# Performance work log

Hardware: AMD Instinct MI355X
Metric: run time of the kernel (lower is better)

## Reference

```python
import jax, jax.numpy as jnp
import numpy as np
from jax import lax

FPLANE = 64
T = 8          # num_segments
HEADS = 4
EPS = 1e-5


def _conv2d(x, w, b):
    # x: [N,C,H,W], w: [O,I,kh,kw]
    y = lax.conv_general_dilated(x, w, (1, 1), 'SAME',
                                 dimension_numbers=('NCHW', 'OIHW', 'NCHW'))
    return y + b[None, :, None, None]


def _conv3d_grouped(x, w, b, groups):
    # x: [N,C,D,H,W], w: [O, C//groups, kd,kh,kw]
    y = lax.conv_general_dilated(x, w, (1, 1, 1), 'SAME',
                                 dimension_numbers=('NCDHW', 'OIDHW', 'NCDHW'),
                                 feature_group_count=groups)
    return y + b[None, :, None, None, None]


def setup_inputs() -> dict:
    key = jax.random.key(0)
    ks = jax.random.split(key, 5)
    N, C, H, W = T * 16, FPLANE, 56, 56
    x = jax.random.normal(ks[0], (N, C, H, W), dtype=jnp.float32)
    attn_w = jax.random.normal(ks[1], (HEADS, C, 3, 3), dtype=jnp.float32) * 0.05
    attn_b = jax.random.normal(ks[2], (HEADS,), dtype=jnp.float32) * 0.05
    bn_gamma = jnp.ones((C,), dtype=jnp.float32)
    bn_beta = jnp.zeros((C,), dtype=jnp.float32)
    conv3d_w = jax.random.normal(ks[3], (2, C // 2, 3, 3, 3), dtype=jnp.float32) * 0.05
    conv3d_b = jax.random.normal(ks[4], (2,), dtype=jnp.float32) * 0.05
    return {'x': x, 'attn_w': attn_w, 'attn_b': attn_b,
            'bn_gamma': bn_gamma, 'bn_beta': bn_beta,
            'conv3d_w': conv3d_w, 'conv3d_b': conv3d_b}


def reference(x, attn_w, attn_b, bn_gamma, bn_beta, conv3d_w, conv3d_b):
    N, C, H, W = x.shape
    B = N // T
    half = C // 2
    quarter = C // 4

    # spatial attention: conv2d -> ReLU -> Sigmoid, per-head gating
    attn = jax.nn.sigmoid(jax.nn.relu(_conv2d(x, attn_w, attn_b)))  # [N,HEADS,H,W]
    xh = x.reshape(N, HEADS, C // HEADS, H, W) * attn[:, :, None]
    x2 = xh.reshape(N, C, H, W)

    # [B*T,C,H,W] -> [B,C,T,H,W]
    x5 = x2.reshape(B, T, C, H, W).transpose(0, 2, 1, 3, 4)

    # BatchNorm3d (training-mode batch statistics) + ReLU
    mean = jnp.mean(x5, axis=(0, 2, 3, 4), keepdims=True)
    var = jnp.var(x5, axis=(0, 2, 3, 4), keepdims=True)
    x_bn = (x5 - mean) * lax.rsqrt(var + EPS)
    x_bn = x_bn * bn_gamma[None, :, None, None, None] + bn_beta[None, :, None, None, None]
    x_bn_relu = jax.nn.relu(x_bn)

    # grouped conv3d gate (2 groups, 1 output channel each), tanh
    gate = jnp.tanh(_conv3d_grouped(x_bn_relu, conv3d_w, conv3d_b, groups=2))  # [B,2,T,H,W]
    g1 = gate[:, 0:1]
    g2 = gate[:, 1:2]

    x_g1 = x5[:, :half]
    x_g2 = x5[:, half:]
    y1 = g1 * x_g1
    y2 = g2 * x_g2
    r1 = x_g1 - y1
    r2 = x_g2 - y2

    pad_t = ((0, 0), (0, 0), (0, 1), (0, 0), (0, 0))
    pad_b = ((0, 0), (0, 0), (1, 0), (0, 0), (0, 0))
    y1 = jnp.pad(y1[:, :, 1:], pad_t) + r1   # left shift in time, zero pad
    y2 = jnp.pad(y2[:, :, :-1], pad_b) + r2  # right shift in time, zero pad

    # interleave sub-halves: view [B,2,C/4,T,H,W] -> permute -> [B,C/2,T,H,W]
    def interleave(y):
        return (y.reshape(B, 2, quarter, T, H, W)
                 .transpose(0, 2, 1, 3, 4, 5)
                 .reshape(B, half, T, H, W))

    y = jnp.concatenate([interleave(y1), interleave(y2)], axis=1)  # [B,C,T,H,W]
    return y.transpose(0, 2, 1, 3, 4).reshape(N, C, H, W)
```

## Files before the change

kernel.cpp:

```cpp
#include <hip/hip_runtime.h>
#include <hip/hip_bf16.h>

#define HW 3136
#define CTOT 64
#define NTOT 128
#define BB 16
#define TTT 8

static __device__ __forceinline__ float bf2f(unsigned short u) {
    union { unsigned int ui; float f; } v;
    v.ui = ((unsigned int)u) << 16;
    return v.f;
}
static __device__ __forceinline__ unsigned short f2bf(float f) {
    union { float f; unsigned int u; } v;
    v.f = f;
    unsigned int u = v.u;
    unsigned int r = (u + 0x7fffu + ((u >> 16) & 1u)) >> 16;
    return (unsigned short)r;
}

__global__ __launch_bounds__(128) void k_attn(const float* __restrict__ x,
                                              const float* __restrict__ aw,
                                              const float* __restrict__ ab,
                                              float* __restrict__ attn,
                                              unsigned short* __restrict__ x2,
                                              float* __restrict__ stats) {
    const int tile = blockIdx.x % 49;
    const int n = blockIdx.x / 49;
    const int chunk = threadIdx.x >> 4;
    const int qi = threadIdx.x & 15;
    const int quad = tile * 16 + qi;
    const int q = quad % 14;
    const int h = quad / 14;
    const int w0 = q * 4;

    __shared__ float wl[2304];
    __shared__ float l[8][16][17];
    __shared__ float4 abuf[4][16];

    const float* xn = x + (size_t)n * CTOT * HW;
    const int c0 = chunk * 8;

    auto loadrows = [&](int c, float r[3][6]) {
#pragma unroll
        for (int dh = 0; dh < 3; ++dh) {
            const int hh = h + dh - 1;
            const bool v = (hh >= 0) && (hh < 56);
            const float* row = xn + c * HW + (v ? hh : h) * 56 + w0;
            const float m = v ? 1.f : 0.f;
            const float4 mid = *(const float4*)row;
            const float e0 = row[(q > 0) ? -1 : 0] * ((q > 0) ? m : 0.f);
            const float e5 = row[(q < 13) ? 4 : 3] * ((q < 13) ? m : 0.f);
            r[dh][0] = e0;
            r[dh][1] = mid.x * m; r[dh][2] = mid.y * m;
            r[dh][3] = mid.z * m; r[dh][4] = mid.w * m;
            r[dh][5] = e5;
        }
    };

    float bufA[3][6], bufB[3][6];
    loadrows(c0, bufA);

#pragma unroll
    for (int i = 0; i < 18; ++i) {
        const int idx = threadIdx.x + i * 128;
        const int hd = idx & 3;
        const int kw = (idx >> 2) % 3;
        const int dh = (idx / 12) % 3;
        const int c = idx / 36;
        wl[idx] = aw[hd * 576 + c * 9 + dh * 3 + kw];
    }
    __syncthreads();

    float acc[4][4];
#pragma unroll
    for (int hd = 0; hd < 4; ++hd)
#pragma unroll
        for (int j = 0; j < 4; ++j) acc[hd][j] = 0.f;

    float midst[8][4];

#pragma unroll
    for (int i = 0; i < 8; ++i) {
        float (*cur)[6] = (i & 1) ? bufB : bufA;
        float (*nxt)[6] = (i & 1) ? bufA : bufB;
        if (i < 7) loadrows(c0 + i + 1, nxt);

        midst[i][0] = cur[1][1]; midst[i][1] = cur[1][2];
        midst[i][2] = cur[1][3]; midst[i][3] = cur[1][4];

        const int c = c0 + i;
#pragma unroll
        for (int dh = 0; dh < 3; ++dh) {
            const float* wb = &wl[c * 36 + dh * 12];
            const float4 wk0 = *(const float4*)(wb);
            const float4 wk1 = *(const float4*)(wb + 4);
            const float4 wk2 = *(const float4*)(wb + 8);
#pragma unroll
            for (int j = 0; j < 4; ++j) {
                const float a0 = cur[dh][j], a1 = cur[dh][j + 1], a2 = cur[dh][j + 2];
                acc[0][j] = fmaf(a0, wk0.x, fmaf(a1, wk1.x, fmaf(a2, wk2.x, acc[0][j])));
                acc[1][j] = fmaf(a0, wk0.y, fmaf(a1, wk1.y, fmaf(a2, wk2.y, acc[1][j])));
                acc[2][j] = fmaf(a0, wk0.z, fmaf(a1, wk1.z, fmaf(a2, wk2.z, acc[2][j])));
                acc[3][j] = fmaf(a0, wk0.w, fmaf(a1, wk1.w, fmaf(a2, wk2.w, acc[3][j])));
            }
        }
    }

    float* mine = &l[chunk][qi][0];
#pragma unroll
    for (int hd = 0; hd < 4; ++hd)
#pragma unroll
        for (int j = 0; j < 4; ++j) mine[hd * 4 + j] = acc[hd][j];
    __syncthreads();

    if (threadIdx.x < 64) {
        const int hd = threadIdx.x >> 4;
        const int rq = threadIdx.x & 15;
        float s0 = ab[hd], s1 = s0, s2 = s0, s3 = s0;
#pragma unroll
        for (int cch = 0; cch < 8; ++cch) {
            const float* p = &l[cch][rq][hd * 4];
            s0 += p[0]; s1 += p[1]; s2 += p[2]; s3 += p[3];
        }
        float4 o;
        o.x = s0 > 0.f ? 1.f / (1.f + __expf(-s0)) : 0.5f;
        o.y = s1 > 0.f ? 1.f / (1.f + __expf(-s1)) : 0.5f;
        o.z = s2 > 0.f ? 1.f / (1.f + __expf(-s2)) : 0.5f;
        o.w = s3 > 0.f ? 1.f / (1.f + __expf(-s3)) : 0.5f;
        *(float4*)(attn + (size_t)(n * 4 + hd) * HW + (tile * 16 + rq) * 4) = o;
        abuf[hd][rq] = o;
    }
    __syncthreads();

    const int head = chunk >> 1;
    const float4 a4 = abuf[head][qi];
    float s[8], sq[8];
#pragma unroll
    for (int i = 0; i < 8; ++i) {
        const float v0 = midst[i][0] * a4.x;
        const float v1 = midst[i][1] * a4.y;
        const float v2 = midst[i][2] * a4.z;
        const float v3 = midst[i][3] * a4.w;
        ushort4 o;
        o.x = f2bf(v0); o.y = f2bf(v1); o.z = f2bf(v2); o.w = f2bf(v3);
        *(ushort4*)(x2 + (size_t)(n * 64 + c0 + i) * HW + quad * 4) = o;
        s[i] = v0 + v1 + v2 + v3;
        sq[i] = v0 * v0 + v1 * v1 + v2 * v2 + v3 * v3;
    }
#pragma unroll
    for (int i = 0; i < 8; ++i) { mine[i] = s[i]; mine[8 + i] = sq[i]; }
    __syncthreads();
    {
        const int ch2 = threadIdx.x >> 4;
        const int k = threadIdx.x & 15;
        float t = 0.f;
#pragma unroll
        for (int qq = 0; qq < 16; ++qq) t += l[ch2][qq][k];
        const int cc = ch2 * 8 + (k & 7);
        const int rep = blockIdx.x & 15;
        atomicAdd(&stats[rep * 128 + (k >> 3) * 64 + cc], t);
    }
}

__global__ void k_finalize(const float* __restrict__ stats,
                           const float* __restrict__ gamma,
                           const float* __restrict__ beta,
                           float* __restrict__ ss) {
    const int c = threadIdx.x;
    float S = 0.f, Q = 0.f;
#pragma unroll
    for (int r = 0; r < 16; ++r) {
        S += stats[r * 128 + c];
        Q += stats[r * 128 + 64 + c];
    }
    const float cnt = 401408.0f;
    const float mean = S / cnt;
    const float var = Q / cnt - mean * mean;
    const float scale = gamma[c] * rsqrtf(var + 1e-5f);
    ss[c] = scale;
    ss[64 + c] = beta[c] - mean * scale;
}

__global__ __launch_bounds__(128) void k_conv3d(const unsigned short* __restrict__ x2,
                                                const float* __restrict__ ss,
                                                const float* __restrict__ w3,
                                                const float* __restrict__ b3,
                                                float* __restrict__ gate) {
    const int tile = blockIdx.x % 49;
    const int oc = (blockIdx.x / 49) & 1;
    const int b = blockIdx.x / 98;
    const int chunk = threadIdx.x >> 4;
    const int qi = threadIdx.x & 15;
    const int quad = tile * 16 + qi;
    const int q = quad % 14;
    const int h = quad / 14;
    const int w0 = q * 4;

    float acc[8][4];
#pragma unroll
    for (int t = 0; t < 8; ++t)
#pragma unroll
        for (int j = 0; j < 4; ++j) acc[t][j] = 0.f;

    const int ic0 = chunk * 4;
    for (int ic = ic0; ic < ic0 + 4; ++ic) {
        const int c = oc * 32 + ic;
        const float sc = ss[c], sh = ss[64 + c];
        const unsigned short* cbase = x2 + (size_t)(b * 8 * 64 + c) * HW;
        const float* wic = w3 + c * 27;
#pragma unroll
        for (int tt = 0; tt < 8; ++tt) {
            const unsigned short* plane = cbase + (size_t)tt * (64 * HW);
            float f[3][6];
#pragma unroll
            for (int dh = 0; dh < 3; ++dh) {
                const int hh = h + dh - 1;
                const bool vld = (hh >= 0) && (hh < 56);
                const unsigned short* row = plane + (vld ? hh : h) * 56 + w0;
                const float m = vld ? 1.f : 0.f;
                const float mL = (q > 0) ? m : 0.f;
                const float mR = (q < 13) ? m : 0.f;
                const ushort4 mid = *(const ushort4*)row;
                const unsigned short e0 = row[(q > 0) ? -1 : 0];
                const unsigned short e5 = row[(q < 13) ? 4 : 3];
                f[dh][0] = fmaxf(fmaf(bf2f(e0),    sc, sh), 0.f) * mL;
                f[dh][1] = fmaxf(fmaf(bf2f(mid.x), sc, sh), 0.f) * m;
                f[dh][2] = fmaxf(fmaf(bf2f(mid.y), sc, sh), 0.f) * m;
                f[dh][3] = fmaxf(fmaf(bf2f(mid.z), sc, sh), 0.f) * m;
                f[dh][4] = fmaxf(fmaf(bf2f(mid.w), sc, sh), 0.f) * m;
                f[dh][5] = fmaxf(fmaf(bf2f(e5),    sc, sh), 0.f) * mR;
            }
#pragma unroll
            for (int dh = 0; dh < 3; ++dh) {
#pragma unroll
                for (int dt = 0; dt < 3; ++dt) {
                    const int t = tt + 1 - dt;
                    if (t < 0 || t > 7) continue;
                    const float* wp = wic + dt * 9 + dh * 3;
                    const float wa = wp[0], wb = wp[1], wc = wp[2];
                    acc[t][0] = fmaf(f[dh][0], wa, fmaf(f[dh][1], wb, fmaf(f[dh][2], wc, acc[t][0])));
                    acc[t][1] = fmaf(f[dh][1], wa, fmaf(f[dh][2], wb, fmaf(f[dh][3], wc, acc[t][1])));
                    acc[t][2] = fmaf(f[dh][2], wa, fmaf(f[dh][3], wb, fmaf(f[dh][4], wc, acc[t][2])));
                    acc[t][3] = fmaf(f[dh][3], wa, fmaf(f[dh][4], wb, fmaf(f[dh][5], wc, acc[t][3])));
                }
            }
        }
    }

    __shared__ float4 l4[8 * 16 * 9];
    float4* mine = &l4[(chunk * 16 + qi) * 9];
#pragma unroll
    for (int t = 0; t < 8; ++t) {
        float4 v;
        v.x = acc[t][0]; v.y = acc[t][1]; v.z = acc[t][2]; v.w = acc[t][3];
        mine[t] = v;
    }
    __syncthreads();

    const int rt = threadIdx.x >> 4;
    const int rq = threadIdx.x & 15;
    float4 s = l4[(0 * 16 + rq) * 9 + rt];
#pragma unroll
    for (int c = 1; c < 8; ++c) {
        const float4 v = l4[(c * 16 + rq) * 9 + rt];
        s.x += v.x; s.y += v.y; s.z += v.z; s.w += v.w;
    }
    const float bb = b3[oc];
    float4 o;
    o.x = tanhf(s.x + bb);
    o.y = tanhf(s.y + bb);
    o.z = tanhf(s.z + bb);
    o.w = tanhf(s.w + bb);
    const int outquad = tile * 16 + rq;
    *(float4*)(gate + (size_t)((b * 2 + oc) * 8 + rt) * HW + outquad * 4) = o;
}

__global__ __launch_bounds__(448) void k_final(const float* __restrict__ x,
                                               const float* __restrict__ attn,
                                               const float* __restrict__ gate,
                                               float* __restrict__ out) {
    const int hg = blockIdx.x & 1;
    const int h = (blockIdx.x >> 1) % 56;
    const int b = blockIdx.x / 112;
    const int q = threadIdx.x % 14;
    const int col = threadIdx.x / 14;
    const int co = hg * 32 + col;
    const int sp = h * 56 + q * 4;

    int cs;
    if (co < 32) {
        cs = ((co & 1) << 4) | (co >> 1);
    } else {
        const int cc = co - 32;
        cs = 32 + (((cc & 1) << 4) | (cc >> 1));
    }
    const int grp = hg;
    const int head = cs >> 4;

    float4 x2v[8], g[8];
#pragma unroll
    for (int t = 0; t < 8; ++t) {
        const int n = b * 8 + t;
        const float4 xv = *(const float4*)(x + (size_t)(n * 64 + cs) * HW + sp);
        const float4 av = *(const float4*)(attn + (size_t)(n * 4 + head) * HW + sp);
        const float4 gv = *(const float4*)(gate + (size_t)((b * 2 + grp) * 8 + t) * HW + sp);
        x2v[t].x = xv.x * av.x;
        x2v[t].y = xv.y * av.y;
        x2v[t].z = xv.z * av.z;
        x2v[t].w = xv.w * av.w;
        g[t] = gv;
    }
#pragma unroll
    for (int t = 0; t < 8; ++t) {
        float4 o;
        o.x = x2v[t].x * (1.f - g[t].x);
        o.y = x2v[t].y * (1.f - g[t].y);
        o.z = x2v[t].z * (1.f - g[t].z);
        o.w = x2v[t].w * (1.f - g[t].w);
        if (grp == 0) {
            if (t < 7) {
                o.x += x2v[t + 1].x * g[t + 1].x;
                o.y += x2v[t + 1].y * g[t + 1].y;
                o.z += x2v[t + 1].z * g[t + 1].z;
                o.w += x2v[t + 1].w * g[t + 1].w;
            }
        } else {
            if (t > 0) {
                o.x += x2v[t - 1].x * g[t - 1].x;
                o.y += x2v[t - 1].y * g[t - 1].y;
                o.z += x2v[t - 1].z * g[t - 1].z;
                o.w += x2v[t - 1].w * g[t - 1].w;
            }
        }
        *(float4*)(out + (size_t)((b * 8 + t) * 64 + co) * HW + sp) = o;
    }
}

extern "C" void kernel_launch(void* const* d_in, const int* in_sizes, int n_in,
                              void* d_out, int out_size, void* d_ws, size_t ws_size,
                              hipStream_t stream) {
    const float* x = (const float*)d_in[0];
    const float* aw = (const float*)d_in[1];
    const float* ab = (const float*)d_in[2];
    const float* gamma = (const float*)d_in[3];
    const float* beta = (const float*)d_in[4];
    const float* w3 = (const float*)d_in[5];
    const float* b3 = (const float*)d_in[6];
    float* out = (float*)d_out;

    char* ws = (char*)d_ws;
    unsigned short* x2 = (unsigned short*)ws;
    float* attn = (float*)(ws + 51380224);
    float* gate = (float*)(ws + 57802752);
    float* stats = (float*)(ws + 57802752);
    float* ss = (float*)(ws + 61014528);

    hipMemsetAsync(stats, 0, 8192, stream);
    k_attn<<<6272, 128, 0, stream>>>(x, aw, ab, attn, x2, stats);
    k_finalize<<<1, 64, 0, stream>>>(stats, gamma, beta, ss);
    k_conv3d<<<1568, 128, 0, stream>>>(x2, ss, w3, b3, gate);
    k_final<<<1792, 448, 0, stream>>>(x, attn, gate, out);
}
```

Baseline: 391.8 us.

## Fold BN finalize into attn kernel, pre-apply BN+ReLU pass, LDS weights in conv3d

The BN statistics finalize moves into the tail of the attention kernel using a last-block atomic counter, which removes one kernel launch. A new elementwise kernel applies BN scale/shift and ReLU to the bf16 x2 buffer in place, so conv3d reads values that are already normalized. Conv3d then caches its weights in LDS and skips out-of-range rows instead of masking them. The cost is an extra full read and write pass over x2 (about 51 MB) plus a second bf16 rounding of the normalized values, which may not pay back the per-element ALU saved in conv3d.

```diff
diff --git a/kernel.cpp b/kernel.cpp
--- a/kernel.cpp
+++ b/kernel.cpp
@@ -23,9 +23,13 @@
 __global__ __launch_bounds__(128) void k_attn(const float* __restrict__ x,
                                               const float* __restrict__ aw,
                                               const float* __restrict__ ab,
+                                              const float* __restrict__ gamma,
+                                              const float* __restrict__ beta,
                                               float* __restrict__ attn,
                                               unsigned short* __restrict__ x2,
-                                              float* __restrict__ stats) {
+                                              float* __restrict__ stats,
+                                              unsigned int* __restrict__ counter,
+                                              float* __restrict__ ss) {
     const int tile = blockIdx.x % 49;
     const int n = blockIdx.x / 49;
     const int chunk = threadIdx.x >> 4;
@@ -162,29 +166,49 @@
         const int rep = blockIdx.x & 15;
         atomicAdd(&stats[rep * 128 + (k >> 3) * 64 + cc], t);
     }
-}
-
-__global__ void k_finalize(const float* __restrict__ stats,
-                           const float* __restrict__ gamma,
-                           const float* __restrict__ beta,
-                           float* __restrict__ ss) {
-    const int c = threadIdx.x;
-    float S = 0.f, Q = 0.f;
-#pragma unroll
-    for (int r = 0; r < 16; ++r) {
-        S += stats[r * 128 + c];
-        Q += stats[r * 128 + 64 + c];
-    }
-    const float cnt = 401408.0f;
-    const float mean = S / cnt;
-    const float var = Q / cnt - mean * mean;
-    const float scale = gamma[c] * rsqrtf(var + 1e-5f);
-    ss[c] = scale;
-    ss[64 + c] = beta[c] - mean * scale;
+
+    __syncthreads();
+    __shared__ unsigned int winflag;
+    if (threadIdx.x == 0) {
+        __threadfence();
+        winflag = (atomicAdd(counter, 1u) == gridDim.x - 1) ? 1u : 0u;
+    }
+    __syncthreads();
+    if (winflag && threadIdx.x < 64) {
+        const int c = threadIdx.x;
+        float S = 0.f, Q = 0.f;
+#pragma unroll
+        for (int r = 0; r < 16; ++r) {
+            S += atomicAdd(&stats[r * 128 + c], 0.f);
+            Q += atomicAdd(&stats[r * 128 + 64 + c], 0.f);
+        }
+        const float cnt = 401408.0f;
+        const float mean = S / cnt;
+        const float var = Q / cnt - mean * mean;
+        const float scale = gamma[c] * rsqrtf(var + 1e-5f);
+        ss[c] = scale;
+        ss[64 + c] = beta[c] - mean * scale;
+    }
+}
+
+__global__ __launch_bounds__(256) void k_bnr(unsigned int* __restrict__ x2u,
+                                             const float* __restrict__ ss) {
+    const int idx = blockIdx.x * 256 + threadIdx.x;
+    const int plane = idx / 392;
+    const int c = plane & 63;
+    const float sc = ss[c], sh = ss[64 + c];
+    uint4 v = ((const uint4*)x2u)[idx];
+    unsigned int* p = (unsigned int*)&v;
+#pragma unroll
+    for (int i = 0; i < 4; ++i) {
+        const float lo = fmaxf(fmaf(bf2f((unsigned short)(p[i] & 0xffffu)), sc, sh), 0.f);
+        const float hi = fmaxf(fmaf(bf2f((unsigned short)(p[i] >> 16)), sc, sh), 0.f);
+        p[i] = (unsigned int)f2bf(lo) | ((unsigned int)f2bf(hi) << 16);
+    }
+    ((uint4*)x2u)[idx] = v;
 }
 
 __global__ __launch_bounds__(128) void k_conv3d(const unsigned short* __restrict__ x2,
-                                                const float* __restrict__ ss,
                                                 const float* __restrict__ w3,
                                                 const float* __restrict__ b3,
                                                 float* __restrict__ gate) {
@@ -198,6 +222,10 @@
     const int h = quad / 14;
     const int w0 = q * 4;
 
+    __shared__ float wlds[864];
+    for (int i = threadIdx.x; i < 864; i += 128) wlds[i] = w3[oc * 864 + i];
+    __syncthreads();
+
     float acc[8][4];
 #pragma unroll
     for (int t = 0; t < 8; ++t)
@@ -207,43 +235,31 @@
     const int ic0 = chunk * 4;
     for (int ic = ic0; ic < ic0 + 4; ++ic) {
         const int c = oc * 32 + ic;
-        const float sc = ss[c], sh = ss[64 + c];
         const unsigned short* cbase = x2 + (size_t)(b * 8 * 64 + c) * HW;
-        const float* wic = w3 + c * 27;
+        const float* wic = &wlds[ic * 27];
 #pragma unroll
         for (int tt = 0; tt < 8; ++tt) {
             const unsigned short* plane = cbase + (size_t)tt * (64 * HW);
-            float f[3][6];
 #pragma unroll
             for (int dh = 0; dh < 3; ++dh) {
                 const int hh = h + dh - 1;
-                const bool vld = (hh >= 0) && (hh < 56);
-                const unsigned short* row = plane + (vld ? hh : h) * 56 + w0;
-                const float m = vld ? 1.f : 0.f;
-                const float mL = (q > 0) ? m : 0.f;
-                const float mR = (q < 13) ? m : 0.f;
+                if (hh < 0 || hh >= 56) continue;
+                const unsigned short* row = plane + hh * 56 + w0;
                 const ushort4 mid = *(const ushort4*)row;
-                const unsigned short e0 = row[(q > 0) ? -1 : 0];
-                const unsigned short e5 = row[(q < 13) ? 4 : 3];
-                f[dh][0] = fmaxf(fmaf(bf2f(e0),    sc, sh), 0.f) * mL;
-                f[dh][1] = fmaxf(fmaf(bf2f(mid.x), sc, sh), 0.f) * m;
-                f[dh][2] = fmaxf(fmaf(bf2f(mid.y), sc, sh), 0.f) * m;
-                f[dh][3] = fmaxf(fmaf(bf2f(mid.z), sc, sh), 0.f) * m;
-                f[dh][4] = fmaxf(fmaf(bf2f(mid.w), sc, sh), 0.f) * m;
-                f[dh][5] = fmaxf(fmaf(bf2f(e5),    sc, sh), 0.f) * mR;
-            }
-#pragma unroll
-            for (int dh = 0; dh < 3; ++dh) {
+                const float f0 = (q > 0) ? bf2f(row[-1]) : 0.f;
+                const float f1 = bf2f(mid.x), f2 = bf2f(mid.y);
+                const float f3 = bf2f(mid.z), f4 = bf2f(mid.w);
+                const float f5 = (q < 13) ? bf2f(row[4]) : 0.f;
 #pragma unroll
                 for (int dt = 0; dt < 3; ++dt) {
                     const int t = tt + 1 - dt;
                     if (t < 0 || t > 7) continue;
                     const float* wp = wic + dt * 9 + dh * 3;
                     const float wa = wp[0], wb = wp[1], wc = wp[2];
-                    acc[t][0] = fmaf(f[dh][0], wa, fmaf(f[dh][1], wb, fmaf(f[dh][2], wc, acc[t][0])));
-                    acc[t][1] = fmaf(f[dh][1], wa, fmaf(f[dh][2], wb, fmaf(f[dh][3], wc, acc[t][1])));
-                    acc[t][2] = fmaf(f[dh][2], wa, fmaf(f[dh][3], wb, fmaf(f[dh][4], wc, acc[t][2])));
-                    acc[t][3] = fmaf(f[dh][3], wa, fmaf(f[dh][4], wb, fmaf(f[dh][5], wc, acc[t][3])));
+                    acc[t][0] = fmaf(f0, wa, fmaf(f1, wb, fmaf(f2, wc, acc[t][0])));
+                    acc[t][1] = fmaf(f1, wa, fmaf(f2, wb, fmaf(f3, wc, acc[t][1])));
+                    acc[t][2] = fmaf(f2, wa, fmaf(f3, wb, fmaf(f4, wc, acc[t][2])));
+                    acc[t][3] = fmaf(f3, wa, fmaf(f4, wb, fmaf(f5, wc, acc[t][3])));
                 }
             }
         }
@@ -355,11 +371,12 @@
     float* attn = (float*)(ws + 51380224);
     float* gate = (float*)(ws + 57802752);
     float* stats = (float*)(ws + 57802752);
+    unsigned int* counter = (unsigned int*)(ws + 57802752 + 8192);
     float* ss = (float*)(ws + 61014528);
 
-    hipMemsetAsync(stats, 0, 8192, stream);
-    k_attn<<<6272, 128, 0, stream>>>(x, aw, ab, attn, x2, stats);
-    k_finalize<<<1, 64, 0, stream>>>(stats, gamma, beta, ss);
-    k_conv3d<<<1568, 128, 0, stream>>>(x2, ss, w3, b3, gate);
+    hipMemsetAsync(stats, 0, 8196, stream);
+    k_attn<<<6272, 128, 0, stream>>>(x, aw, ab, gamma, beta, attn, x2, stats, counter, ss);
+    k_bnr<<<12544, 256, 0, stream>>>((unsigned int*)x2, ss);
+    k_conv3d<<<1568, 128, 0, stream>>>(x2, w3, b3, gate);
     k_final<<<1792, 448, 0, stream>>>(x, attn, gate, out);
 }
```

Result: slower. 613.0 us (+56.5%).
